# Optimization experiments

Measured on AMD Instinct MI355X. Metric: run time of the kernel, lower is better.

The kernel has to match this reference:

```python
import jax, jax.numpy as jnp
import numpy as np

N = 50000      # nodes
E = 1600000    # edges (avg degree 32)
R = 8          # relation types
G = 64         # graphs in batch
D_IN = 128
HID = 128
CLS = 10


def setup_inputs() -> dict:
    key = jax.random.key(0)
    ks = jax.random.split(key, 12)
    s = 0.05  # weight init scale
    return {
        "x": jax.random.normal(ks[0], (N, D_IN), dtype=jnp.float32),
        "edge_index": jax.random.randint(ks[1], (2, E), 0, N, dtype=jnp.int32),
        "edge_type": jax.random.randint(ks[2], (E,), 0, R, dtype=jnp.int32),
        "batch": jnp.sort(jax.random.randint(ks[3], (N,), 0, G, dtype=jnp.int32)),
        "W1": jax.random.normal(ks[4], (R, D_IN, HID), dtype=jnp.float32) * s,
        "root1": jax.random.normal(ks[5], (D_IN, HID), dtype=jnp.float32) * s,
        "b1": jax.random.normal(ks[6], (HID,), dtype=jnp.float32) * s,
        "W2": jax.random.normal(ks[7], (R, HID, HID), dtype=jnp.float32) * s,
        "root2": jax.random.normal(ks[8], (HID, HID), dtype=jnp.float32) * s,
        "b2": jax.random.normal(ks[9], (HID,), dtype=jnp.float32) * s,
        "lin_w": jax.random.normal(ks[10], (HID, CLS), dtype=jnp.float32) * s,
        "lin_b": jax.random.normal(ks[11], (CLS,), dtype=jnp.float32) * s,
    }


def rgcn_conv(x, edge_index, edge_type, W, root, bias):
    # PyG RGCNConv (default aggr='mean'): per-relation mean of neighbor
    # features, relation-specific matmul, summed over relations, + root + bias.
    src, dst = edge_index[0], edge_index[1]
    d_in = x.shape[1]
    seg = dst * R + edge_type                      # fused (node, relation) segment id
    msg = jax.ops.segment_sum(x[src], seg, num_segments=N * R)          # [N*R, d_in]
    cnt = jax.ops.segment_sum(jnp.ones((E,), x.dtype), seg, num_segments=N * R)
    mean = (msg / jnp.maximum(cnt, 1.0)[:, None]).reshape(N, R, d_in)   # [N, R, d_in]
    return jnp.einsum('nrd,rdh->nh', mean, W) + x @ root + bias


def reference(x, edge_index, edge_type, batch, W1, root1, b1, W2, root2, b2, lin_w, lin_b):
    h = jax.nn.relu(rgcn_conv(x, edge_index, edge_type, W1, root1, b1))
    h = jax.nn.relu(rgcn_conv(h, edge_index, edge_type, W2, root2, b2))
    # global mean pool per graph
    gsum = jax.ops.segment_sum(h, batch, num_segments=G)                # [G, HID]
    gcnt = jax.ops.segment_sum(jnp.ones((N,), h.dtype), batch, num_segments=G)
    g = gsum / jnp.maximum(gcnt, 1.0)[:, None]
    return g @ lin_w + lin_b                                            # [G, CLS]
```

## Files before the change

kernel.cpp:

```cpp
#include <hip/hip_runtime.h>

#define N_NODES 50000
#define N_EDGES 1600000
#define R_REL 8
#define G_GRAPHS 64
#define D_INF 128
#define HIDF 128
#define CLSF 10

#define S_SEG (N_NODES * R_REL)
#define RZ 9
#define PCHUNK 16

#define XG 8
#define NODES_PER_G (N_NODES / XG)
#define SORT_BLKS_PER_G 256
#define SORT_GRID (XG * SORT_BLKS_PER_G)

typedef __attribute__((ext_vector_type(8))) short short8;
typedef __attribute__((ext_vector_type(4))) float floatx4;

typedef __attribute__((address_space(1))) const unsigned int guint;
typedef __attribute__((address_space(3))) unsigned int luint;
__device__ __forceinline__ void gload_lds16(const void* g, void* l) {
    __builtin_amdgcn_global_load_lds((guint*)g, (luint*)l, 16, 0, 0);
}

__device__ __forceinline__ unsigned short f2bf(float f) {
    unsigned int u = __float_as_uint(f);
    unsigned int r = (u + 0x7fffu + ((u >> 16) & 1u)) >> 16;
    return (unsigned short)r;
}
__device__ __forceinline__ float bflo(unsigned int u) { return __uint_as_float(u << 16); }
__device__ __forceinline__ float bfhi(unsigned int u) { return __uint_as_float(u & 0xffff0000u); }

__global__ __launch_bounds__(256) void count_kernel(const int* __restrict__ dst,
                                                    const int* __restrict__ et,
                                                    int* __restrict__ cnt) {
    int xg = blockIdx.x & (XG - 1);
    int inner = blockIdx.x >> 3;
    int lo = xg * NODES_PER_G, hi = lo + NODES_PER_G;
    for (int e = inner * 256 + threadIdx.x; e < N_EDGES; e += SORT_BLKS_PER_G * 256) {
        int d = dst[e];
        if (d >= lo && d < hi) {
            atomicAdd(&cnt[d * R_REL + et[e]], 1);
        }
    }
}

#define SCAN_BLK 256
#define SCAN_ELEMS 1024
#define NB_SCAN ((S_SEG + SCAN_ELEMS - 1) / SCAN_ELEMS)

__global__ __launch_bounds__(SCAN_BLK) void scan1_kernel(const int* __restrict__ cnt,
                                                         int* __restrict__ off,
                                                         int* __restrict__ bsum) {
    __shared__ int sd[SCAN_BLK];
    int t = threadIdx.x;
    int base = blockIdx.x * SCAN_ELEMS + t * 4;
    int v[4];
    int tsum = 0;
#pragma unroll
    for (int j = 0; j < 4; j++) {
        v[j] = (base + j < S_SEG) ? cnt[base + j] : 0;
        tsum += v[j];
    }
    sd[t] = tsum;
    __syncthreads();
    for (int d = 1; d < SCAN_BLK; d <<= 1) {
        int x = (t >= d) ? sd[t - d] : 0;
        __syncthreads();
        sd[t] += x;
        __syncthreads();
    }
    int incl = sd[t];
    int run = incl - tsum;
#pragma unroll
    for (int j = 0; j < 4; j++) {
        if (base + j < S_SEG) off[base + j] = run;
        run += v[j];
    }
    if (t == SCAN_BLK - 1) bsum[blockIdx.x] = incl;
}

__global__ __launch_bounds__(512) void scan2_kernel(int* __restrict__ bsum) {
    __shared__ int sd[512];
    int t = threadIdx.x;
    int v = (t < NB_SCAN) ? bsum[t] : 0;
    sd[t] = v;
    __syncthreads();
    for (int d = 1; d < 512; d <<= 1) {
        int x = (t >= d) ? sd[t - d] : 0;
        __syncthreads();
        sd[t] += x;
        __syncthreads();
    }
    if (t < NB_SCAN) bsum[t] = sd[t] - v;
}

__global__ void absoff_kernel(int* __restrict__ off, const int* __restrict__ bsum,
                              const int* __restrict__ cnt, float* __restrict__ winv,
                              int* __restrict__ cursor) {
    int i = blockIdx.x * blockDim.x + threadIdx.x;
    if (i < S_SEG) {
        int v = off[i] + bsum[i >> 10];
        off[i] = v;
        cursor[i] = v;
        winv[i] = 1.0f / (float)max(cnt[i], 1);
    }
}

__global__ __launch_bounds__(256) void bin_kernel(const int* __restrict__ src,
                                                  const int* __restrict__ dst,
                                                  const int* __restrict__ et,
                                                  int* __restrict__ cursor,
                                                  int* __restrict__ zidx) {
    int xg = blockIdx.x & (XG - 1);
    int inner = blockIdx.x >> 3;
    int lo = xg * NODES_PER_G, hi = lo + NODES_PER_G;
    for (int e = inner * 256 + threadIdx.x; e < N_EDGES; e += SORT_BLKS_PER_G * 256) {
        int d = dst[e];
        if (d >= lo && d < hi) {
            int t = et[e];
            int seg = d * R_REL + t;
            int pos = atomicAdd(&cursor[seg], 1);
            zidx[pos] = ((src[e] * RZ + t) << 7) | t;
        }
    }
}

__global__ void convx_kernel(const float* __restrict__ x, unsigned short* __restrict__ xb) {
    int idx = blockIdx.x * blockDim.x + threadIdx.x;
    if (idx < N_NODES * D_INF) xb[idx] = f2bf(x[idx]);
}

__global__ __launch_bounds__(256) void convw9_kernel(const float* __restrict__ W,
                                                     const float* __restrict__ root,
                                                     unsigned short* __restrict__ wz) {
    __shared__ float t[16][17];
    int r = blockIdx.z;
    int k0 = blockIdx.x * 16, c0 = blockIdx.y * 16;
    int tx = threadIdx.x & 15, ty = threadIdx.x >> 4;
    const float* srcp = (r < 8) ? (W + (size_t)r * 128 * 128) : root;
    t[ty][tx] = srcp[(size_t)(k0 + ty) * 128 + c0 + tx];
    __syncthreads();
    wz[(size_t)r * 16384 + (size_t)(c0 + ty) * 128 + k0 + tx] = f2bf(t[tx][ty]);
}

__global__ __launch_bounds__(256) void transform_gemm(
    const unsigned short* __restrict__ hb,
    const unsigned short* __restrict__ wz,
    unsigned short* __restrict__ z)
{
    __shared__ __align__(16) unsigned short A4[4][64][32];
    __shared__ __align__(16) unsigned short B4[4][128][32];

    const int tx = threadIdx.x;
    const int wave = tx >> 6, lane = tx & 63;
    const int quad = lane >> 4, lq = lane & 15;
    const int row0 = blockIdx.x * 64;
    const int srow = lane >> 2;
    const int sch  = lane & 3;

#pragma unroll
    for (int kk = 0; kk < 4; kk++) {
        int gr = row0 + wave * 16 + srow; if (gr >= N_NODES) gr = N_NODES - 1;
        gload_lds16(hb + (size_t)gr * HIDF + kk * 32 + sch * 8, &A4[kk][wave * 16][0]);
    }

    floatx4 acc[8];
    for (int r = 0; r < RZ; r++) {
#pragma unroll
        for (int kk = 0; kk < 4; kk++) {
#pragma unroll
            for (int p = 0; p < 2; p++) {
                int cc = (wave * 2 + p) * 16;
                gload_lds16(wz + ((size_t)r * 128 + cc + srow) * 128 + kk * 32 + sch * 8,
                            &B4[kk][cc][0]);
            }
        }
        __syncthreads();

#pragma unroll
        for (int j = 0; j < 8; j++) acc[j] = (floatx4){0.f, 0.f, 0.f, 0.f};
#pragma unroll
        for (int kk = 0; kk < 4; kk++) {
            short8 af = *(const short8*)(&A4[kk][wave * 16 + lq][quad * 8]);
#pragma unroll
            for (int j = 0; j < 8; j++) {
                short8 bfr = *(const short8*)(&B4[kk][j * 16 + lq][quad * 8]);
                acc[j] = __builtin_amdgcn_mfma_f32_16x16x32_bf16(af, bfr, acc[j], 0, 0, 0);
            }
        }

#pragma unroll
        for (int j = 0; j < 8; j++) {
            int col = j * 16 + lq;
#pragma unroll
            for (int rg = 0; rg < 4; rg++) {
                int row = row0 + wave * 16 + quad * 4 + rg;
                if (row < N_NODES)
                    z[((size_t)row * RZ + r) * 128 + col] = f2bf(acc[j][rg]);
            }
        }
        __syncthreads();
    }
}

__global__ __launch_bounds__(256) void agg2_kernel(const unsigned short* __restrict__ z,
                                                   const int* __restrict__ zidx,
                                                   const float* __restrict__ winv,
                                                   const int* __restrict__ off,
                                                   const float* __restrict__ bias,
                                                   unsigned short* __restrict__ hout) {
    __shared__ float swinv[64];
    int nod0 = blockIdx.x * 8;
    if (threadIdx.x < 64) {
        int idx = nod0 * R_REL + threadIdx.x;
        swinv[threadIdx.x] = (idx < S_SEG) ? winv[idx] : 1.0f;
    }
    __syncthreads();

    int hw = threadIdx.x >> 5;
    int nod = nod0 + hw;
    if (nod >= N_NODES) return;
    int c = threadIdx.x & 31;
    int beg = off[nod * R_REL];
    int end = (nod < N_NODES - 1) ? off[(nod + 1) * R_REL] : N_EDGES;
    const float* wl = &swinv[hw * 8];

    float a0 = 0.f, a1 = 0.f, a2 = 0.f, a3 = 0.f;
    int e = beg;
    for (; e + 4 <= end; e += 4) {
        int p0 = zidx[e + 0], p1 = zidx[e + 1], p2 = zidx[e + 2], p3 = zidx[e + 3];
        float w0 = wl[p0 & 7], w1 = wl[p1 & 7], w2 = wl[p2 & 7], w3 = wl[p3 & 7];
        uint2 v0 = *(const uint2*)(z + (size_t)(p0 & 0x7FFFFF80) + c * 4);
        uint2 v1 = *(const uint2*)(z + (size_t)(p1 & 0x7FFFFF80) + c * 4);
        uint2 v2 = *(const uint2*)(z + (size_t)(p2 & 0x7FFFFF80) + c * 4);
        uint2 v3 = *(const uint2*)(z + (size_t)(p3 & 0x7FFFFF80) + c * 4);
        a0 += bflo(v0.x) * w0 + bflo(v1.x) * w1 + bflo(v2.x) * w2 + bflo(v3.x) * w3;
        a1 += bfhi(v0.x) * w0 + bfhi(v1.x) * w1 + bfhi(v2.x) * w2 + bfhi(v3.x) * w3;
        a2 += bflo(v0.y) * w0 + bflo(v1.y) * w1 + bflo(v2.y) * w2 + bflo(v3.y) * w3;
        a3 += bfhi(v0.y) * w0 + bfhi(v1.y) * w1 + bfhi(v2.y) * w2 + bfhi(v3.y) * w3;
    }
    for (; e < end; e++) {
        int p = zidx[e];
        float w = wl[p & 7];
        uint2 v = *(const uint2*)(z + (size_t)(p & 0x7FFFFF80) + c * 4);
        a0 += bflo(v.x) * w; a1 += bfhi(v.x) * w;
        a2 += bflo(v.y) * w; a3 += bfhi(v.y) * w;
    }
    uint2 vr = *(const uint2*)(z + ((size_t)nod * RZ + 8) * 128 + c * 4);
    a0 += bflo(vr.x); a1 += bfhi(vr.x); a2 += bflo(vr.y); a3 += bfhi(vr.y);
    float4 b = *(const float4*)(bias + c * 4);
    a0 = fmaxf(a0 + b.x, 0.0f);
    a1 = fmaxf(a1 + b.y, 0.0f);
    a2 = fmaxf(a2 + b.z, 0.0f);
    a3 = fmaxf(a3 + b.w, 0.0f);
    uint2 o;
    o.x = (unsigned int)f2bf(a0) | ((unsigned int)f2bf(a1) << 16);
    o.y = (unsigned int)f2bf(a2) | ((unsigned int)f2bf(a3) << 16);
    *(uint2*)(hout + (size_t)nod * HIDF + c * 4) = o;
}

__global__ __launch_bounds__(256) void pool1_kernel(const unsigned short* __restrict__ h,
                                                    const int* __restrict__ batch,
                                                    float* __restrict__ partial) {
    int g = blockIdx.x;
    int p = blockIdx.y;
    int lo, hi;
    {
        int l = 0, r = N_NODES;
        while (l < r) { int m = (l + r) >> 1; if (batch[m] < g) l = m + 1; else r = m; }
        lo = l;
        l = lo; r = N_NODES;
        while (l < r) { int m = (l + r) >> 1; if (batch[m] < g + 1) l = m + 1; else r = m; }
        hi = l;
    }
    int t = threadIdx.x;
    int rowlane = t >> 5;
    int c4 = t & 31;
    float a0 = 0.f, a1 = 0.f, a2 = 0.f, a3 = 0.f;
    for (int n = lo + p + rowlane * PCHUNK; n < hi; n += 8 * PCHUNK) {
        uint2 v = *(const uint2*)(h + (size_t)n * HIDF + c4 * 4);
        a0 += bflo(v.x); a1 += bfhi(v.x); a2 += bflo(v.y); a3 += bfhi(v.y);
    }
    __shared__ float red[8][128];
    if (rowlane == 0) {
        red[0][c4 * 4 + 0] = a0; red[0][c4 * 4 + 1] = a1;
        red[0][c4 * 4 + 2] = a2; red[0][c4 * 4 + 3] = a3;
    }
    __syncthreads();
    for (int s = 1; s < 8; s++) {
        if (rowlane == s) {
            red[0][c4 * 4 + 0] += a0; red[0][c4 * 4 + 1] += a1;
            red[0][c4 * 4 + 2] += a2; red[0][c4 * 4 + 3] += a3;
        }
        __syncthreads();
    }
    if (t < 128) partial[((size_t)g * PCHUNK + p) * 128 + t] = red[0][t];
}

__global__ __launch_bounds__(128) void pool2_kernel(const float* __restrict__ partial,
                                                    const int* __restrict__ batch,
                                                    float* __restrict__ gmean) {
    int g = blockIdx.x;
    int lo, hi;
    {
        int l = 0, r = N_NODES;
        while (l < r) { int m = (l + r) >> 1; if (batch[m] < g) l = m + 1; else r = m; }
        lo = l;
        l = lo; r = N_NODES;
        while (l < r) { int m = (l + r) >> 1; if (batch[m] < g + 1) l = m + 1; else r = m; }
        hi = l;
    }
    int t = threadIdx.x;
    float s = 0.f;
#pragma unroll
    for (int p = 0; p < PCHUNK; p++)
        s += partial[((size_t)g * PCHUNK + p) * 128 + t];
    gmean[g * HIDF + t] = s / (float)max(hi - lo, 1);
}

__global__ void final_kernel(const float* __restrict__ gmean,
                             const float* __restrict__ lin_w,
                             const float* __restrict__ lin_b,
                             float* __restrict__ out) {
    __shared__ float gl[HIDF];
    int g = blockIdx.x;
    int hh = threadIdx.x;
    gl[hh] = gmean[g * HIDF + hh];
    __syncthreads();
    if (hh < CLSF) {
        float s = lin_b[hh];
#pragma unroll 16
        for (int d = 0; d < HIDF; d++) s += gl[d] * lin_w[d * CLSF + hh];
        out[g * CLSF + hh] = s;
    }
}

extern "C" void kernel_launch(void* const* d_in, const int* in_sizes, int n_in,
                              void* d_out, int out_size, void* d_ws, size_t ws_size,
                              hipStream_t stream) {
    const float* x     = (const float*)d_in[0];
    const int*   ei    = (const int*)d_in[1];
    const int*   et    = (const int*)d_in[2];
    const int*   batch = (const int*)d_in[3];
    const float* W1    = (const float*)d_in[4];
    const float* root1 = (const float*)d_in[5];
    const float* b1    = (const float*)d_in[6];
    const float* W2    = (const float*)d_in[7];
    const float* root2 = (const float*)d_in[8];
    const float* b2    = (const float*)d_in[9];
    const float* lin_w = (const float*)d_in[10];
    const float* lin_b = (const float*)d_in[11];
    float* out = (float*)d_out;

    const int* src = ei;
    const int* dst = ei + N_EDGES;

    char* ws = (char*)d_ws;
    unsigned short* xb  = (unsigned short*)ws; ws += (size_t)N_NODES * HIDF * 2;
    unsigned short* h1  = (unsigned short*)ws; ws += (size_t)N_NODES * HIDF * 2;
    unsigned short* h2  = (unsigned short*)ws; ws += (size_t)N_NODES * HIDF * 2;
    unsigned short* z   = (unsigned short*)ws; ws += (size_t)N_NODES * RZ * 128 * 2;
    unsigned short* wz1 = (unsigned short*)ws; ws += (size_t)RZ * 128 * 128 * 2;
    unsigned short* wz2 = (unsigned short*)ws; ws += (size_t)RZ * 128 * 128 * 2;
    int*   cnt    = (int*)ws;   ws += (size_t)S_SEG * 4;
    int*   off    = (int*)ws;   ws += (size_t)S_SEG * 4;
    int*   bsum   = (int*)ws;   ws += 512 * 4;
    int*   cursor = (int*)ws;   ws += (size_t)S_SEG * 4;
    float* winv   = (float*)ws; ws += (size_t)S_SEG * 4;
    int*   zidx   = (int*)ws;   ws += (size_t)N_EDGES * 4;
    float* partial = (float*)ws; ws += (size_t)G_GRAPHS * PCHUNK * 128 * 4;
    float* gmean  = (float*)ws; ws += (size_t)G_GRAPHS * HIDF * 4;

    hipMemsetAsync(cnt, 0, (size_t)S_SEG * 4, stream);

    count_kernel<<<SORT_GRID, 256, 0, stream>>>(dst, et, cnt);
    scan1_kernel<<<NB_SCAN, SCAN_BLK, 0, stream>>>(cnt, off, bsum);
    scan2_kernel<<<1, 512, 0, stream>>>(bsum);
    absoff_kernel<<<(S_SEG + 255) / 256, 256, 0, stream>>>(off, bsum, cnt, winv, cursor);
    bin_kernel<<<SORT_GRID, 256, 0, stream>>>(src, dst, et, cursor, zidx);

    convx_kernel<<<(N_NODES * D_INF + 255) / 256, 256, 0, stream>>>(x, xb);
    convw9_kernel<<<dim3(8, 8, RZ), 256, 0, stream>>>(W1, root1, wz1);
    convw9_kernel<<<dim3(8, 8, RZ), 256, 0, stream>>>(W2, root2, wz2);

    const int NGB = (N_NODES + 63) / 64;
    const int NAB = (N_NODES + 7) / 8;

    transform_gemm<<<NGB, 256, 0, stream>>>(xb, wz1, z);
    agg2_kernel<<<NAB, 256, 0, stream>>>(z, zidx, winv, off, b1, h1);

    transform_gemm<<<NGB, 256, 0, stream>>>(h1, wz2, z);
    agg2_kernel<<<NAB, 256, 0, stream>>>(z, zidx, winv, off, b2, h2);

    pool1_kernel<<<dim3(G_GRAPHS, PCHUNK), 256, 0, stream>>>(h2, batch, partial);
    pool2_kernel<<<G_GRAPHS, 128, 0, stream>>>(partial, batch, gmean);
    final_kernel<<<G_GRAPHS, HIDF, 0, stream>>>(gmean, lin_w, lin_b, out);

    (void)in_sizes; (void)n_in; (void)out_size; (void)ws_size;
}
```

Baseline: 498.0 us.

## Double transform GEMM row tile to 128 and stream B per k-chunk

The transform GEMM now gives each block 128 node rows instead of 64, so each wave computes a 32x128 output tile and every loaded weight fragment is reused across two A fragments. B is staged one 32-wide k-chunk at a time into a smaller LDS buffer, with barriers around each chunk. The aim is to halve how often the weight matrices are reloaded per node and raise MFMA work per LDS read. The cost is more barriers per relation, larger accumulator register use, and half as many blocks (about 391) on a GPU with many CUs.

```diff
diff --git a/kernel.cpp b/kernel.cpp
--- a/kernel.cpp
+++ b/kernel.cpp
@@ -152,58 +152,71 @@
     const unsigned short* __restrict__ wz,
     unsigned short* __restrict__ z)
 {
-    __shared__ __align__(16) unsigned short A4[4][64][32];
-    __shared__ __align__(16) unsigned short B4[4][128][32];
+    __shared__ __align__(16) unsigned short A4[4][128][32];
+    __shared__ __align__(16) unsigned short Bc[128][32];
 
     const int tx = threadIdx.x;
     const int wave = tx >> 6, lane = tx & 63;
     const int quad = lane >> 4, lq = lane & 15;
-    const int row0 = blockIdx.x * 64;
+    const int row0 = blockIdx.x * 128;
     const int srow = lane >> 2;
     const int sch  = lane & 3;
 
 #pragma unroll
     for (int kk = 0; kk < 4; kk++) {
-        int gr = row0 + wave * 16 + srow; if (gr >= N_NODES) gr = N_NODES - 1;
-        gload_lds16(hb + (size_t)gr * HIDF + kk * 32 + sch * 8, &A4[kk][wave * 16][0]);
-    }
-
-    floatx4 acc[8];
+#pragma unroll
+        for (int p = 0; p < 2; p++) {
+            int rr = (wave * 2 + p) * 16;
+            int gr = row0 + rr + srow; if (gr >= N_NODES) gr = N_NODES - 1;
+            gload_lds16(hb + (size_t)gr * HIDF + kk * 32 + sch * 8, &A4[kk][rr][0]);
+        }
+    }
+
+    floatx4 acc[2][8];
     for (int r = 0; r < RZ; r++) {
+#pragma unroll
+        for (int i = 0; i < 2; i++)
+#pragma unroll
+            for (int j = 0; j < 8; j++) acc[i][j] = (floatx4){0.f, 0.f, 0.f, 0.f};
+
 #pragma unroll
         for (int kk = 0; kk < 4; kk++) {
 #pragma unroll
             for (int p = 0; p < 2; p++) {
                 int cc = (wave * 2 + p) * 16;
                 gload_lds16(wz + ((size_t)r * 128 + cc + srow) * 128 + kk * 32 + sch * 8,
-                            &B4[kk][cc][0]);
+                            &Bc[cc][0]);
             }
-        }
-        __syncthreads();
-
-#pragma unroll
-        for (int j = 0; j < 8; j++) acc[j] = (floatx4){0.f, 0.f, 0.f, 0.f};
-#pragma unroll
-        for (int kk = 0; kk < 4; kk++) {
-            short8 af = *(const short8*)(&A4[kk][wave * 16 + lq][quad * 8]);
+            __syncthreads();
+
+            short8 af[2], bfr[8];
+#pragma unroll
+            for (int i = 0; i < 2; i++)
+                af[i] = *(const short8*)(&A4[kk][wave * 32 + i * 16 + lq][quad * 8]);
+#pragma unroll
+            for (int j = 0; j < 8; j++)
+                bfr[j] = *(const short8*)(&Bc[j * 16 + lq][quad * 8]);
+#pragma unroll
+            for (int i = 0; i < 2; i++)
+#pragma unroll
+                for (int j = 0; j < 8; j++)
+                    acc[i][j] = __builtin_amdgcn_mfma_f32_16x16x32_bf16(af[i], bfr[j], acc[i][j], 0, 0, 0);
+            __syncthreads();
+        }
+
+#pragma unroll
+        for (int i = 0; i < 2; i++) {
 #pragma unroll
             for (int j = 0; j < 8; j++) {
-                short8 bfr = *(const short8*)(&B4[kk][j * 16 + lq][quad * 8]);
-                acc[j] = __builtin_amdgcn_mfma_f32_16x16x32_bf16(af, bfr, acc[j], 0, 0, 0);
+                int col = j * 16 + lq;
+#pragma unroll
+                for (int rg = 0; rg < 4; rg++) {
+                    int row = row0 + wave * 32 + i * 16 + quad * 4 + rg;
+                    if (row < N_NODES)
+                        z[((size_t)row * RZ + r) * 128 + col] = f2bf(acc[i][j][rg]);
+                }
             }
         }
-
-#pragma unroll
-        for (int j = 0; j < 8; j++) {
-            int col = j * 16 + lq;
-#pragma unroll
-            for (int rg = 0; rg < 4; rg++) {
-                int row = row0 + wave * 16 + quad * 4 + rg;
-                if (row < N_NODES)
-                    z[((size_t)row * RZ + r) * 128 + col] = f2bf(acc[j][rg]);
-            }
-        }
-        __syncthreads();
     }
 }
 
@@ -387,7 +400,7 @@
     convw9_kernel<<<dim3(8, 8, RZ), 256, 0, stream>>>(W1, root1, wz1);
     convw9_kernel<<<dim3(8, 8, RZ), 256, 0, stream>>>(W2, root2, wz2);
 
-    const int NGB = (N_NODES + 63) / 64;
+    const int NGB = (N_NODES + 127) / 128;
     const int NAB = (N_NODES + 7) / 8;
 
     transform_gemm<<<NGB, 256, 0, stream>>>(xb, wz1, z);
```

Result: no change. 490.1 us (-1.6%).
